# Kernel optimization log

Hardware: AMD Instinct MI355X
Metric: run time of the kernel (lower is better)

The kernel has to match this reference:

```python
import jax, jax.numpy as jnp
import numpy as np

BS, V, N, C_IN, C_OUT = 8, 4096, 16, 64, 64


def setup_inputs() -> dict:
    key = jax.random.key(0)
    k1, k2, k3, k4, k5 = jax.random.split(key, 5)
    stdv = 1.0 / np.sqrt(N * C_IN)
    return {
        "neighbor_index": jax.random.randint(k1, (BS, V, N), 0, V, dtype=jnp.int64),
        "vertices": jax.random.normal(k2, (BS, V, 3), dtype=jnp.float32),
        "feature_map": jax.random.normal(k3, (BS, V, C_IN), dtype=jnp.float32),
        "weights": jax.random.uniform(k4, (C_OUT, (N + 1) * C_IN), dtype=jnp.float32, minval=-stdv, maxval=stdv),
        "bias": jax.random.uniform(k5, (C_OUT,), dtype=jnp.float32, minval=-stdv, maxval=stdv),
    }


def reference(neighbor_index, vertices, feature_map, weights, bias):
    bs, v, n = neighbor_index.shape
    # gather neighbor features per batch element: (bs, v, n, c)
    neighbors = jax.vmap(lambda f, idx: f[idx])(feature_map, neighbor_index)
    # prepend self feature: (bs, v, n+1, c)
    feats = jnp.concatenate([feature_map[:, :, None, :], neighbors], axis=2)
    # torch permutes to (bs, c, n+1, v) then reshapes -> flat index = c*(n+1)+k,
    # equivalent to transposing last two dims here before flattening
    flat = feats.transpose(0, 1, 3, 2).reshape(bs, v, -1)  # (bs, v, c*(n+1))
    out = jnp.einsum('bvf,of->bvo', flat, weights) + bias
    return jax.nn.relu(out)
```

## Files before the change

kernel.cpp:

```cpp
#include <hip/hip_runtime.h>
#include <stdint.h>

#define NV 4096

typedef __attribute__((ext_vector_type(8))) short bf16x8;
typedef __attribute__((ext_vector_type(4))) float f32x4;

__device__ __forceinline__ unsigned short f2bf(float f) {
  union { float f; unsigned int u; } v; v.f = f;
  unsigned int r = v.u + 0x7FFF + ((v.u >> 16) & 1);
  return (unsigned short)(r >> 16);
}

__global__ __launch_bounds__(256)
void prep(const float* __restrict__ fm, const float* __restrict__ w,
          unsigned short* __restrict__ fmb, unsigned short* __restrict__ wb) {
  int blk = blockIdx.x;
  if (blk < 1024) {
    int i = (blk * 256 + threadIdx.x) * 8;
    float4 v0 = *(const float4*)(fm + i);
    float4 v1 = *(const float4*)(fm + i + 4);
    ushort4 o0, o1;
    o0.x = f2bf(v0.x); o0.y = f2bf(v0.y); o0.z = f2bf(v0.z); o0.w = f2bf(v0.w);
    o1.x = f2bf(v1.x); o1.y = f2bf(v1.y); o1.z = f2bf(v1.z); o1.w = f2bf(v1.w);
    *(ushort4*)(fmb + i) = o0;
    *(ushort4*)(fmb + i + 4) = o1;
  } else {
    int t = (blk - 1024) * 256 + threadIdx.x;
    int c = t & 63;
    int o = (t >> 6) & 63;
    int k = t >> 12;
    wb[t] = f2bf(w[o * 1088 + c * 17 + k]);
  }
}

__global__ __launch_bounds__(512, 2)
void conv_main(const int* __restrict__ nbr, const unsigned short* __restrict__ fmb,
               const unsigned short* __restrict__ wb, const float* __restrict__ bias,
               float* __restrict__ out) {
  __shared__ unsigned char smem[73728];

  const int bid = blockIdx.x;
  const int b = bid & 7;
  const int tile = bid >> 3;
  const int tid = threadIdx.x;
  const int lane = tid & 63;
  const int lm = lane & 15;
  const int lk = lane >> 4;
  const int w8 = tid >> 6;
  const int rg = w8 >> 1;
  const int h = w8 & 1;

  const int rbase = tile * 128;
  const bf16x8* fb8 = (const bf16x8*)(fmb + (size_t)b * NV * 64);

  const int r0 = tid >> 3;
  const int c8 = tid & 7;
  const int swz = c8 ^ (r0 & 7);
  const int row0g = rbase + r0;
  const int row1g = rbase + r0 + 64;

  const int4* q0 = (const int4*)(nbr + ((size_t)b * NV + row0g) * 16);
  const int4* q1 = (const int4*)(nbr + ((size_t)b * NV + row1g) * 16);
  const int4 i0a = q0[0], i0b = q0[1], i0c = q0[2], i0d = q0[3];
  const int4 i1a = q1[0], i1b = q1[1], i1c = q1[2], i1d = q1[3];

  const int fsl = h * 4 + lk;
  const int offW = lm * 128 + ((fsl ^ (lm & 7)) << 4);
  const int rowL0 = rg * 32 + lm;
  const int rowL1 = rg * 32 + 16 + lm;
  const int offA0 = rowL0 * 128 + ((fsl ^ (rowL0 & 7)) << 4);
  const int offA1 = rowL1 * 128 + ((fsl ^ (rowL1 & 7)) << 4);

  f32x4 accA0{0,0,0,0}, accA1{0,0,0,0}, accA2{0,0,0,0}, accA3{0,0,0,0};
  f32x4 accB0{0,0,0,0}, accB1{0,0,0,0}, accB2{0,0,0,0}, accB3{0,0,0,0};

#define SBR __builtin_amdgcn_sched_barrier(0)
#define MFMA __builtin_amdgcn_mfma_f32_16x16x32_bf16

#define STAGE(SLOT, BUF, SVA, SVB) {                                        \
    {                                                                       \
      int o_ = (tid >> 3) & 63, s_ = tid & 7;                               \
      const unsigned short* ws_ =                                           \
          wb + (SLOT) * 4096 + o_ * 64 + ((s_ ^ (o_ & 7)) << 3);            \
      __builtin_amdgcn_global_load_lds(                                     \
          (const __attribute__((address_space(1))) void*)ws_,               \
          (__attribute__((address_space(3))) void*)(smem + (BUF) * 8192 + tid * 16), \
          16, 0, 0);                                                        \
    }                                                                       \
    {                                                                       \
      const bf16x8* fa_ = fb8 + (size_t)(SVA) * 8 + swz;                    \
      __builtin_amdgcn_global_load_lds(                                     \
          (const __attribute__((address_space(1))) void*)fa_,               \
          (__attribute__((address_space(3))) void*)(smem + 24576 + (BUF) * 16384 + tid * 16), \
          16, 0, 0);                                                        \
      const bf16x8* fbp_ = fb8 + (size_t)(SVB) * 8 + swz;                   \
      __builtin_amdgcn_global_load_lds(                                     \
          (const __attribute__((address_space(1))) void*)fbp_,              \
          (__attribute__((address_space(3))) void*)(smem + 24576 + (BUF) * 16384 + 8192 + tid * 16), \
          16, 0, 0);                                                        \
    }                                                                       \
  }

#define CONSUME(BUF) {                                                     \
    const unsigned char* wp_ = smem + (BUF) * 8192;                        \
    const unsigned char* fp_ = smem + 24576 + (BUF) * 16384;               \
    bf16x8 W0 = *(const bf16x8*)(wp_ + 0 * 2048 + offW);                   \
    bf16x8 W1 = *(const bf16x8*)(wp_ + 1 * 2048 + offW);                   \
    bf16x8 W2 = *(const bf16x8*)(wp_ + 2 * 2048 + offW);                   \
    bf16x8 W3 = *(const bf16x8*)(wp_ + 3 * 2048 + offW);                   \
    bf16x8 A0 = *(const bf16x8*)(fp_ + offA0);                             \
    bf16x8 A1 = *(const bf16x8*)(fp_ + offA1);                             \
    accA0 = MFMA(A0, W0, accA0, 0, 0, 0);                                  \
    accA1 = MFMA(A0, W1, accA1, 0, 0, 0);                                  \
    accA2 = MFMA(A0, W2, accA2, 0, 0, 0);                                  \
    accA3 = MFMA(A0, W3, accA3, 0, 0, 0);                                  \
    accB0 = MFMA(A1, W0, accB0, 0, 0, 0);                                  \
    accB1 = MFMA(A1, W1, accB1, 0, 0, 0);                                  \
    accB2 = MFMA(A1, W2, accB2, 0, 0, 0);                                  \
    accB3 = MFMA(A1, W3, accB3, 0, 0, 0);                                  \
  }

#define WAITBAR(N)                                                          \
    SBR; asm volatile("s_waitcnt vmcnt(" #N ")" ::: "memory"); SBR;         \
    __builtin_amdgcn_s_barrier(); SBR;

  STAGE(0, 0, row0g, row1g); SBR;
  STAGE(1, 1, i0a.x, i1a.x); SBR;
  WAITBAR(3);

  STAGE(2, 2, i0a.y, i1a.y);  SBR; CONSUME(0); WAITBAR(3);
  STAGE(3, 0, i0a.z, i1a.z);  SBR; CONSUME(1); WAITBAR(3);
  STAGE(4, 1, i0a.w, i1a.w);  SBR; CONSUME(2); WAITBAR(3);
  STAGE(5, 2, i0b.x, i1b.x);  SBR; CONSUME(0); WAITBAR(3);
  STAGE(6, 0, i0b.y, i1b.y);  SBR; CONSUME(1); WAITBAR(3);
  STAGE(7, 1, i0b.z, i1b.z);  SBR; CONSUME(2); WAITBAR(3);
  STAGE(8, 2, i0b.w, i1b.w);  SBR; CONSUME(0); WAITBAR(3);
  STAGE(9, 0, i0c.x, i1c.x);  SBR; CONSUME(1); WAITBAR(3);
  STAGE(10, 1, i0c.y, i1c.y); SBR; CONSUME(2); WAITBAR(3);
  STAGE(11, 2, i0c.z, i1c.z); SBR; CONSUME(0); WAITBAR(3);
  STAGE(12, 0, i0c.w, i1c.w); SBR; CONSUME(1); WAITBAR(3);
  STAGE(13, 1, i0d.x, i1d.x); SBR; CONSUME(2); WAITBAR(3);
  STAGE(14, 2, i0d.y, i1d.y); SBR; CONSUME(0); WAITBAR(3);
  STAGE(15, 0, i0d.z, i1d.z); SBR; CONSUME(1); WAITBAR(3);
  STAGE(16, 1, i0d.w, i1d.w); SBR; CONSUME(2); WAITBAR(3);
  CONSUME(0); WAITBAR(0);
  CONSUME(1);

#undef WAITBAR
#undef CONSUME
#undef STAGE
#undef MFMA
#undef SBR

  __syncthreads();
  if (h == 1) {
    float* rp = (float*)smem + rg * 2048 + lane * 4;
    *(f32x4*)(rp + 0 * 256) = accA0;
    *(f32x4*)(rp + 1 * 256) = accA1;
    *(f32x4*)(rp + 2 * 256) = accA2;
    *(f32x4*)(rp + 3 * 256) = accA3;
    *(f32x4*)(rp + 4 * 256) = accB0;
    *(f32x4*)(rp + 5 * 256) = accB1;
    *(f32x4*)(rp + 6 * 256) = accB2;
    *(f32x4*)(rp + 7 * 256) = accB3;
  }
  __syncthreads();
  if (h == 0) {
    const float* rp = (const float*)smem + rg * 2048 + lane * 4;
    accA0 += *(const f32x4*)(rp + 0 * 256);
    accA1 += *(const f32x4*)(rp + 1 * 256);
    accA2 += *(const f32x4*)(rp + 2 * 256);
    accA3 += *(const f32x4*)(rp + 3 * 256);
    accB0 += *(const f32x4*)(rp + 4 * 256);
    accB1 += *(const f32x4*)(rp + 5 * 256);
    accB2 += *(const f32x4*)(rp + 6 * 256);
    accB3 += *(const f32x4*)(rp + 7 * 256);

    const float bv0 = bias[lm];
    const float bv1 = bias[16 + lm];
    const float bv2 = bias[32 + lm];
    const float bv3 = bias[48 + lm];
    float* op = out + (size_t)b * NV * 64;
    #pragma unroll
    for (int mt = 0; mt < 2; ++mt) {
      const int gv = rbase + rg * 32 + mt * 16 + lk * 4;
      #pragma unroll
      for (int r = 0; r < 4; ++r) {
        float* orow = op + (size_t)(gv + r) * 64;
        if (mt == 0) {
          orow[lm]      = fmaxf(accA0[r] + bv0, 0.f);
          orow[16 + lm] = fmaxf(accA1[r] + bv1, 0.f);
          orow[32 + lm] = fmaxf(accA2[r] + bv2, 0.f);
          orow[48 + lm] = fmaxf(accA3[r] + bv3, 0.f);
        } else {
          orow[lm]      = fmaxf(accB0[r] + bv0, 0.f);
          orow[16 + lm] = fmaxf(accB1[r] + bv1, 0.f);
          orow[32 + lm] = fmaxf(accB2[r] + bv2, 0.f);
          orow[48 + lm] = fmaxf(accB3[r] + bv3, 0.f);
        }
      }
    }
  }
}

extern "C" void kernel_launch(void* const* d_in, const int* in_sizes, int n_in,
                              void* d_out, int out_size, void* d_ws, size_t ws_size,
                              hipStream_t stream) {
  const int* nbr = (const int*)d_in[0];
  const float* fm = (const float*)d_in[2];
  const float* w = (const float*)d_in[3];
  const float* bias = (const float*)d_in[4];
  float* out = (float*)d_out;

  unsigned short* fmb = (unsigned short*)d_ws;
  unsigned short* wb = fmb + (size_t)8 * NV * 64;

  prep<<<1296, 256, 0, stream>>>(fm, w, fmb, wb);
  conv_main<<<256, 512, 0, stream>>>(nbr, fmb, wb, bias, out);
}
```

Baseline: 19.75 us.

## Deepen LDS pipeline to six buffers with two stages per barrier

Grows LDS from three to six stage buffers (147 KB) and issues two neighbor slots per iteration, consuming two stages between barriers. This halves the number of barrier/waitcnt points and keeps more gather loads in flight to hide latency. In exchange, launch bounds drop to one block per CU, so occupancy halves and latency hiding relies on the deeper prefetch alone.

```diff
diff --git a/kernel.cpp b/kernel.cpp
--- a/kernel.cpp
+++ b/kernel.cpp
@@ -34,11 +34,11 @@
   }
 }
 
-__global__ __launch_bounds__(512, 2)
+__global__ __launch_bounds__(512, 1)
 void conv_main(const int* __restrict__ nbr, const unsigned short* __restrict__ fmb,
                const unsigned short* __restrict__ wb, const float* __restrict__ bias,
                float* __restrict__ out) {
-  __shared__ unsigned char smem[73728];
+  __shared__ unsigned char smem[147456];
 
   const int bid = blockIdx.x;
   const int b = bid & 7;
@@ -92,19 +92,19 @@
       const bf16x8* fa_ = fb8 + (size_t)(SVA) * 8 + swz;                    \
       __builtin_amdgcn_global_load_lds(                                     \
           (const __attribute__((address_space(1))) void*)fa_,               \
-          (__attribute__((address_space(3))) void*)(smem + 24576 + (BUF) * 16384 + tid * 16), \
+          (__attribute__((address_space(3))) void*)(smem + 49152 + (BUF) * 16384 + tid * 16), \
           16, 0, 0);                                                        \
       const bf16x8* fbp_ = fb8 + (size_t)(SVB) * 8 + swz;                   \
       __builtin_amdgcn_global_load_lds(                                     \
           (const __attribute__((address_space(1))) void*)fbp_,              \
-          (__attribute__((address_space(3))) void*)(smem + 24576 + (BUF) * 16384 + 8192 + tid * 16), \
+          (__attribute__((address_space(3))) void*)(smem + 49152 + (BUF) * 16384 + 8192 + tid * 16), \
           16, 0, 0);                                                        \
     }                                                                       \
   }
 
 #define CONSUME(BUF) {                                                     \
     const unsigned char* wp_ = smem + (BUF) * 8192;                        \
-    const unsigned char* fp_ = smem + 24576 + (BUF) * 16384;               \
+    const unsigned char* fp_ = smem + 49152 + (BUF) * 16384;               \
     bf16x8 W0 = *(const bf16x8*)(wp_ + 0 * 2048 + offW);                   \
     bf16x8 W1 = *(const bf16x8*)(wp_ + 1 * 2048 + offW);                   \
     bf16x8 W2 = *(const bf16x8*)(wp_ + 2 * 2048 + offW);                   \
@@ -125,27 +125,26 @@
     SBR; asm volatile("s_waitcnt vmcnt(" #N ")" ::: "memory"); SBR;         \
     __builtin_amdgcn_s_barrier(); SBR;
 
-  STAGE(0, 0, row0g, row1g); SBR;
-  STAGE(1, 1, i0a.x, i1a.x); SBR;
-  WAITBAR(3);
-
-  STAGE(2, 2, i0a.y, i1a.y);  SBR; CONSUME(0); WAITBAR(3);
-  STAGE(3, 0, i0a.z, i1a.z);  SBR; CONSUME(1); WAITBAR(3);
-  STAGE(4, 1, i0a.w, i1a.w);  SBR; CONSUME(2); WAITBAR(3);
-  STAGE(5, 2, i0b.x, i1b.x);  SBR; CONSUME(0); WAITBAR(3);
-  STAGE(6, 0, i0b.y, i1b.y);  SBR; CONSUME(1); WAITBAR(3);
-  STAGE(7, 1, i0b.z, i1b.z);  SBR; CONSUME(2); WAITBAR(3);
-  STAGE(8, 2, i0b.w, i1b.w);  SBR; CONSUME(0); WAITBAR(3);
-  STAGE(9, 0, i0c.x, i1c.x);  SBR; CONSUME(1); WAITBAR(3);
-  STAGE(10, 1, i0c.y, i1c.y); SBR; CONSUME(2); WAITBAR(3);
-  STAGE(11, 2, i0c.z, i1c.z); SBR; CONSUME(0); WAITBAR(3);
-  STAGE(12, 0, i0c.w, i1c.w); SBR; CONSUME(1); WAITBAR(3);
-  STAGE(13, 1, i0d.x, i1d.x); SBR; CONSUME(2); WAITBAR(3);
-  STAGE(14, 2, i0d.y, i1d.y); SBR; CONSUME(0); WAITBAR(3);
-  STAGE(15, 0, i0d.z, i1d.z); SBR; CONSUME(1); WAITBAR(3);
-  STAGE(16, 1, i0d.w, i1d.w); SBR; CONSUME(2); WAITBAR(3);
-  CONSUME(0); WAITBAR(0);
-  CONSUME(1);
+  STAGE(0, 0, row0g, row1g);   STAGE(1, 1, i0a.x, i1a.x);  SBR;
+  STAGE(2, 2, i0a.y, i1a.y);   STAGE(3, 3, i0a.z, i1a.z);  SBR;
+  WAITBAR(6);
+
+  STAGE(4, 4, i0a.w, i1a.w);   STAGE(5, 5, i0b.x, i1b.x);  SBR;
+  CONSUME(0); CONSUME(1);      WAITBAR(6);
+  STAGE(6, 0, i0b.y, i1b.y);   STAGE(7, 1, i0b.z, i1b.z);  SBR;
+  CONSUME(2); CONSUME(3);      WAITBAR(6);
+  STAGE(8, 2, i0b.w, i1b.w);   STAGE(9, 3, i0c.x, i1c.x);  SBR;
+  CONSUME(4); CONSUME(5);      WAITBAR(6);
+  STAGE(10, 4, i0c.y, i1c.y);  STAGE(11, 5, i0c.z, i1c.z); SBR;
+  CONSUME(0); CONSUME(1);      WAITBAR(6);
+  STAGE(12, 0, i0c.w, i1c.w);  STAGE(13, 1, i0d.x, i1d.x); SBR;
+  CONSUME(2); CONSUME(3);      WAITBAR(6);
+  STAGE(14, 2, i0d.y, i1d.y);  STAGE(15, 3, i0d.z, i1d.z); SBR;
+  CONSUME(4); CONSUME(5);      WAITBAR(6);
+  STAGE(16, 4, i0d.w, i1d.w);  SBR;
+  CONSUME(0); CONSUME(1);      WAITBAR(3);
+  CONSUME(2); CONSUME(3);      WAITBAR(0);
+  CONSUME(4);
 
 #undef WAITBAR
 #undef CONSUME
```

Result: faster. 19.24 us (-2.6%).
